# Performance work log

Hardware: AMD Instinct MI355X
Metric: run time of the kernel (lower is better)

The kernel has to match this reference:

```python
import jax, jax.numpy as jnp
import numpy as np

HEADS = 8
DIM_HEAD = 64
C = 512              # in_channels == inner_dim = heads*dim_head
WIN = 7              # window size implied by rel_pos table (2*7-1 = 13)
EPS = 1e-5


def setup_inputs() -> dict:
    key = jax.random.key(0)
    ks = jax.random.split(key, 6)
    B = 2048
    inner = HEADS * DIM_HEAD
    x = jax.random.normal(ks[0], (B, C, WIN, WIN), dtype=jnp.float32)
    gamma = jnp.ones((C,), dtype=jnp.float32)
    beta = jnp.zeros((C,), dtype=jnp.float32)
    w_qkv = jax.random.normal(ks[1], (C, 3 * inner), dtype=jnp.float32) / np.sqrt(C)
    rel_table = jax.random.normal(ks[2], (2 * WIN - 1, 2 * WIN - 1, HEADS), dtype=jnp.float32)
    w_out = jax.random.normal(ks[3], (inner, C), dtype=jnp.float32) / np.sqrt(inner)
    b_out = jnp.zeros((C,), dtype=jnp.float32)
    return {"x": x, "gamma": gamma, "beta": beta, "w_qkv": w_qkv,
            "rel_table": rel_table, "w_out": w_out, "b_out": b_out}


def _rel_pos_bias(rel_table, H, W):
    # Swin-style additive bias: bias[h, i, j] = table[hi-hj+H-1, wi-wj+W-1, h]
    hh = jnp.arange(H)
    ww = jnp.arange(W)
    hi = jnp.repeat(hh, W)          # [N] row index of each flattened position
    wi = jnp.tile(ww, H)            # [N] col index
    dh = hi[:, None] - hi[None, :] + (H - 1)   # [N, N]
    dw = wi[:, None] - wi[None, :] + (W - 1)   # [N, N]
    bias = rel_table[dh, dw]        # [N, N, heads]
    return jnp.transpose(bias, (2, 0, 1))      # [heads, N, N]


def reference(x, gamma, beta, w_qkv, rel_table, w_out, b_out):
    B, Cc, H, W = x.shape
    N = H * W
    shortcut = x
    xs = jnp.transpose(x.reshape(B, Cc, N), (0, 2, 1))   # [B, N, C]
    # LayerNorm over channel dim
    mu = jnp.mean(xs, axis=-1, keepdims=True)
    var = jnp.var(xs, axis=-1, keepdims=True)
    xn = (xs - mu) * jax.lax.rsqrt(var + EPS) * gamma + beta
    qkv = xn @ w_qkv                                      # [B, N, 3*inner]
    q, k, v = jnp.split(qkv, 3, axis=-1)
    def heads(t):
        return jnp.transpose(t.reshape(B, N, HEADS, DIM_HEAD), (0, 2, 1, 3))  # [B,h,N,d]
    q, k, v = heads(q), heads(k), heads(v)
    scale = DIM_HEAD ** -0.5
    dots = jnp.einsum('bhnd,bhmd->bhnm', q, k) * scale   # [B,h,N,N]
    dots = dots + _rel_pos_bias(rel_table, H, W)[None]   # add Swin-style bias
    attn = jax.nn.softmax(dots, axis=-1)
    out = jnp.einsum('bhnm,bhmd->bhnd', attn, v)         # [B,h,N,d]
    out = jnp.transpose(out, (0, 2, 1, 3)).reshape(B, N, HEADS * DIM_HEAD)
    out = out @ w_out + b_out                            # [B, N, C]
    out = jnp.transpose(out, (0, 2, 1)).reshape(B, Cc, H, W)
    return out + shortcut
```

## Files before the change

### kernel.cpp

```cpp
#include <hip/hip_runtime.h>

#define BATCH 2048
#define CH 512
#define NTOK 49
#define NHEAD 8
#define DHEAD 64

typedef __attribute__((ext_vector_type(8))) short bf16x8;
typedef __attribute__((ext_vector_type(4))) float f32x4;

__device__ __forceinline__ ushort f2bf(float f) {
  union { float f; unsigned u; } v; v.f = f;
  unsigned r = v.u + 0x7fffu + ((v.u >> 16) & 1u);
  return (ushort)(r >> 16);
}

__device__ __forceinline__ float bf2f(ushort u) {
  union { unsigned u; float f; } v; v.u = ((unsigned)u) << 16;
  return v.f;
}

#define MFMA16(a, b, c) __builtin_amdgcn_mfma_f32_16x16x32_bf16((a), (b), (c), 0, 0, 0)

#define GLOAD_LDS16(gsrc, ldst)                                                  \
  __builtin_amdgcn_global_load_lds((const __attribute__((address_space(1))) void*)(gsrc), \
                                   (__attribute__((address_space(3))) void*)(ldst), 16, 0, 0)

__global__ void prep_kernel(const float* __restrict__ w_qkv, const float* __restrict__ w_out,
                            const float* __restrict__ rel, ushort* __restrict__ wqkvB,
                            ushort* __restrict__ woutF, float* __restrict__ biasF) {
  int tid = blockIdx.x * blockDim.x + threadIdx.x;
  int stride = gridDim.x * blockDim.x;
  for (int i = tid; i < 12 * 16 * 8 * 64 * 8; i += stride) {
    int j = i & 7, lane = (i >> 3) & 63, cbs = (i >> 9) & 7, kk = (i >> 12) & 15, nb = i >> 16;
    int o = nb * 128 + cbs * 16 + (lane & 15);
    int c = kk * 32 + (lane >> 4) * 8 + j;
    wqkvB[i] = f2bf(w_qkv[c * 1536 + o]);
  }
  for (int i = tid; i < 32 * 16 * 64 * 8; i += stride) {
    int j = i & 7, lane = (i >> 3) & 63, ks = (i >> 9) & 15, cb = i >> 13;
    int o = cb * 16 + (lane & 15);
    int c = ks * 32 + (lane >> 4) * 8 + j;
    woutF[i] = f2bf(w_out[c * 512 + o]);
  }
  for (int i = tid; i < NHEAD * 4 * 4 * 64; i += stride) {
    int lane = i & 63, nt = (i >> 6) & 3, mt = (i >> 8) & 3, h = i >> 10;
    int cc = lane & 15, g = lane >> 4;
    float4 v;
#pragma unroll
    for (int r = 0; r < 4; r++) {
      int n = mt * 16 + 4 * g + r;
      int m = nt * 16 + cc;
      float bv = -1e30f;
      if (n < NTOK && m < NTOK) {
        int dh = n / 7 - m / 7 + 6;
        int dw = n % 7 - m % 7 + 6;
        bv = rel[(dh * 13 + dw) * 8 + h];
      }
      ((float*)&v)[r] = bv;
    }
    ((float4*)biasF)[i] = v;
  }
}

__global__ __launch_bounds__(256) void ln_kernel(const float* __restrict__ x,
                                                 const float* __restrict__ gamma,
                                                 const float* __restrict__ beta,
                                                 ushort* __restrict__ xnW) {
  int b = blockIdx.x;
  int t = threadIdx.x;
  __shared__ ushort xsb[CH][NTOK];
  __shared__ float muL[64], rsL[64];
  const float4* x4 = (const float4*)(x + (size_t)b * CH * NTOK);
  for (int i4 = t; i4 < CH * NTOK / 4; i4 += 256) {
    float4 v = x4[i4];
    int lf = i4 * 4;
#pragma unroll
    for (int e = 0; e < 4; e++) {
      int idx = lf + e;
      int c = idx / NTOK, n = idx - c * NTOK;
      xsb[c][n] = f2bf(((const float*)&v)[e]);
    }
  }
  __syncthreads();
  int row = t >> 2, sub = t & 3;
  float s = 0.f, s2 = 0.f;
  if (row < NTOK) {
    for (int c = sub; c < CH; c += 4) {
      float v = bf2f(xsb[c][row]);
      s += v;
      s2 += v * v;
    }
  }
  s += __shfl_xor(s, 1);
  s += __shfl_xor(s, 2);
  s2 += __shfl_xor(s2, 1);
  s2 += __shfl_xor(s2, 2);
  if (sub == 0 && row < NTOK) {
    float m = s * (1.f / CH);
    muL[row] = m;
    rsL[row] = rsqrtf(s2 * (1.f / CH) - m * m + 1e-5f);
  }
  __syncthreads();
  ushort* dst = xnW + (size_t)b * NTOK * CH;
  for (int i = t; i < NTOK * 64; i += 256) {
    int n = i >> 6, c0 = (i & 63) * 8;
    float mu = muL[n], rs = rsL[n];
    ushort tmp[8];
#pragma unroll
    for (int j = 0; j < 8; j++) {
      int c = c0 + j;
      tmp[j] = f2bf((bf2f(xsb[c][n]) - mu) * rs * gamma[c] + beta[c]);
    }
    *(uint4*)(dst + (size_t)n * CH + c0) = *(const uint4*)tmp;
  }
}

__global__ __launch_bounds__(256, 4) void qkv_gemm(const ushort* __restrict__ xnW,
                                                   const ushort* __restrict__ wqkvB,
                                                   ushort* __restrict__ qW,
                                                   ushort* __restrict__ kW,
                                                   ushort* __restrict__ vW) {
  int bid = blockIdx.x;
  int f = (bid & 7) * 1176 + (bid >> 3);
  int mb = f / 12, nb = f - mb * 12;
  int r0 = mb * 128;
  int t = threadIdx.x, lane = t & 63, w = t >> 6;
  int wm = w >> 1, wn = w & 1;

  __shared__ __align__(16) ushort lds[16384];

  const int arow = lane & 15, g = lane >> 4;
  const ushort* wBbase = wqkvB + (size_t)nb * 16 * 4096;
  const ushort* xbase = xnW + (size_t)r0 * CH;

  int drow = t >> 3;
  int slot = t & 7;
  int gchunk = slot ^ (drow & 7);

#pragma unroll
  for (int i = 0; i < 4; i++) {
    int row = drow + i * 32;
    GLOAD_LDS16(xbase + (size_t)row * CH + gchunk * 8, lds + i * 2048 + t * 8);
  }
  __syncthreads();

  f32x4 acc[4][4];
#pragma unroll
  for (int mt = 0; mt < 4; mt++)
#pragma unroll
    for (int nt = 0; nt < 4; nt++) acc[mt][nt] = (f32x4){0.f, 0.f, 0.f, 0.f};

  int cur = 0;
  for (int stage = 0; stage < 8; ++stage) {
    if (stage < 7) {
      int nxt = cur ^ 1, kk = stage + 1;
#pragma unroll
      for (int i = 0; i < 4; i++) {
        GLOAD_LDS16(xbase + (size_t)(drow + i * 32) * CH + kk * 64 + gchunk * 8,
                    lds + nxt * 8192 + i * 2048 + t * 8);
      }
    }
    const ushort* lA = lds + cur * 8192;
#pragma unroll
    for (int ks = 0; ks < 2; ks++) {
      int kk2 = stage * 2 + ks;
      const ushort* wp = wBbase + (size_t)kk2 * 4096 + (wn * 4) * 512 + lane * 8;
      bf16x8 bfr[4];
#pragma unroll
      for (int nt = 0; nt < 4; nt++) bfr[nt] = *(const bf16x8*)(wp + nt * 512);
      bf16x8 afr[4];
#pragma unroll
      for (int mt = 0; mt < 4; mt++) {
        int row = wm * 64 + mt * 16 + arow;
        afr[mt] = *(const bf16x8*)&lA[row * 64 + ((ks * 4 + g) ^ (arow & 7)) * 8];
      }
#pragma unroll
      for (int mt = 0; mt < 4; mt++)
#pragma unroll
        for (int nt = 0; nt < 4; nt++) acc[mt][nt] = MFMA16(afr[mt], bfr[nt], acc[mt][nt]);
    }
    __syncthreads();
    cur ^= 1;
  }

  ushort(*oL)[136] = (ushort(*)[136])lds;
  int h0 = (nb & 3) * 2;
  int sct = nb >> 2;
  float sc = (sct == 0) ? 0.125f : 1.0f;
#pragma unroll
  for (int hh = 0; hh < 2; hh++) {
    if (wm == hh) {
#pragma unroll
      for (int mt = 0; mt < 4; mt++)
#pragma unroll
        for (int nt = 0; nt < 4; nt++)
#pragma unroll
          for (int r = 0; r < 4; r++) {
            int rn = mt * 16 + 4 * g + r;
            oL[rn][wn * 64 + nt * 16 + arow] = f2bf(acc[mt][nt][r] * sc);
          }
    }
    __syncthreads();
    if (sct < 2) {
      ushort* dst = (sct == 0 ? qW : kW);
      for (int i = t; i < 64 * 16; i += 256) {
        int rn = i >> 4, c8 = i & 15;
        int grow = r0 + hh * 64 + rn;
        int b = grow / 49, n = grow - b * 49;
        int h = h0 + (c8 >> 3);
        *(uint4*)(dst + (size_t)(b * 8 + h) * (NTOK * 64) + n * 64 + (c8 & 7) * 8) =
            *(const uint4*)&oL[rn][c8 * 8];
      }
    } else {
      for (int i = t; i < 64 * 128; i += 256) {
        int rn = i & 63, col = i >> 6;
        int grow = r0 + hh * 64 + rn;
        int b = grow / 49, n = grow - b * 49;
        int h = h0 + (col >> 6), d = col & 63;
        vW[(size_t)(b * 8 + h) * 4096 + d * 64 + n] = oL[rn][col];
      }
    }
    __syncthreads();
  }
}

__global__ __launch_bounds__(512, 3) void attnproj(const ushort* __restrict__ qW,
                                                   const ushort* __restrict__ kW,
                                                   const ushort* __restrict__ vW,
                                                   const float* __restrict__ biasF,
                                                   const ushort* __restrict__ woutF,
                                                   const float* __restrict__ b_out,
                                                   const float* __restrict__ x,
                                                   float* __restrict__ out) {
  int b = blockIdx.x;
  int t = threadIdx.x;
  int lane = t & 63;
  int w = t >> 6;

  __shared__ __align__(16) ushort lds[25480];
  ushort* plb = lds + w * 3136;

  const int c = lane & 15, g = lane >> 4;
  const ushort* qb = qW + (size_t)(b * 8 + w) * NTOK * 64;
  const ushort* kb = kW + (size_t)(b * 8 + w) * NTOK * 64;
  const ushort* vb = vW + (size_t)(b * 8 + w) * 64 * 64;
  const float4* bf = (const float4*)biasF + (size_t)w * 16 * 64;

  f32x4 s[4][4];
#pragma unroll
  for (int mt = 0; mt < 4; mt++)
#pragma unroll
    for (int nt = 0; nt < 4; nt++) s[mt][nt] = (f32x4){0.f, 0.f, 0.f, 0.f};
  __builtin_amdgcn_s_setprio(1);
#pragma unroll
  for (int ks = 0; ks < 2; ks++) {
    bf16x8 kf[4];
#pragma unroll
    for (int nt = 0; nt < 4; nt++)
      kf[nt] = *(const bf16x8*)(kb + (size_t)(nt * 16 + c) * 64 + ks * 32 + g * 8);
#pragma unroll
    for (int mt = 0; mt < 4; mt++) {
      bf16x8 qf = *(const bf16x8*)(qb + (size_t)(mt * 16 + c) * 64 + ks * 32 + g * 8);
#pragma unroll
      for (int nt = 0; nt < 4; nt++) s[mt][nt] = MFMA16(qf, kf[nt], s[mt][nt]);
    }
  }
  __builtin_amdgcn_s_setprio(0);

#pragma unroll
  for (int mt = 0; mt < 4; mt++)
#pragma unroll
    for (int nt = 0; nt < 4; nt++) {
      float4 bb = bf[(mt * 4 + nt) * 64 + lane];
#pragma unroll
      for (int r = 0; r < 4; r++) s[mt][nt][r] += ((const float*)&bb)[r];
    }

#pragma unroll
  for (int mt = 0; mt < 4; mt++)
#pragma unroll
    for (int r = 0; r < 4; r++) {
      float mx = fmaxf(fmaxf(s[mt][0][r], s[mt][1][r]), fmaxf(s[mt][2][r], s[mt][3][r]));
      mx = fmaxf(mx, __shfl_xor(mx, 1));
      mx = fmaxf(mx, __shfl_xor(mx, 2));
      mx = fmaxf(mx, __shfl_xor(mx, 4));
      mx = fmaxf(mx, __shfl_xor(mx, 8));
      float p0 = __expf(s[mt][0][r] - mx);
      float p1 = __expf(s[mt][1][r] - mx);
      float p2 = __expf(s[mt][2][r] - mx);
      float p3 = __expf(s[mt][3][r] - mx);
      float sum = p0 + p1 + p2 + p3;
      sum += __shfl_xor(sum, 1);
      sum += __shfl_xor(sum, 2);
      sum += __shfl_xor(sum, 4);
      sum += __shfl_xor(sum, 8);
      float rinv = 1.f / sum;
      int n = mt * 16 + 4 * g + r;
      if (n < NTOK) {
        int n7 = n & 7;
        int chi = c >> 3, clo = c & 7;
        plb[n * 64 + ((0 + chi) ^ n7) * 8 + clo] = f2bf(p0 * rinv);
        plb[n * 64 + ((2 + chi) ^ n7) * 8 + clo] = f2bf(p1 * rinv);
        plb[n * 64 + ((4 + chi) ^ n7) * 8 + clo] = f2bf(p2 * rinv);
        plb[n * 64 + ((6 + chi) ^ n7) * 8 + clo] = f2bf(p3 * rinv);
      }
    }

  f32x4 o[4][4];
#pragma unroll
  for (int mt = 0; mt < 4; mt++)
#pragma unroll
    for (int nt = 0; nt < 4; nt++) o[mt][nt] = (f32x4){0.f, 0.f, 0.f, 0.f};
  __builtin_amdgcn_s_setprio(1);
#pragma unroll
  for (int ks = 0; ks < 2; ks++) {
    bf16x8 vf[4];
#pragma unroll
    for (int nt = 0; nt < 4; nt++)
      vf[nt] = *(const bf16x8*)(vb + (size_t)(nt * 16 + c) * 64 + ks * 32 + g * 8);
#pragma unroll
    for (int mt = 0; mt < 4; mt++) {
      int row = mt * 16 + c;
      int rr = row < NTOK ? row : 48;
      bf16x8 pf = *(const bf16x8*)&plb[rr * 64 + ((ks * 4 + g) ^ (rr & 7)) * 8];
#pragma unroll
      for (int nt = 0; nt < 4; nt++) o[mt][nt] = MFMA16(pf, vf[nt], o[mt][nt]);
    }
  }
  __builtin_amdgcn_s_setprio(0);

  bf16x8 bcur[4];
#pragma unroll
  for (int nt = 0; nt < 4; nt++)
    bcur[nt] = *(const bf16x8*)(woutF + ((size_t)((w * 4 + nt) * 16 + 0)) * 512 + lane * 8);

  __syncthreads();

  ushort(*aoL)[520] = (ushort(*)[520])lds;
#pragma unroll
  for (int mt = 0; mt < 4; mt++)
#pragma unroll
    for (int nt = 0; nt < 4; nt++)
#pragma unroll
      for (int r = 0; r < 4; r++) {
        int n = mt * 16 + 4 * g + r;
        if (n < NTOK) aoL[n][w * 64 + nt * 16 + c] = f2bf(o[mt][nt][r]);
      }
  __syncthreads();

  f32x4 pacc[4][4];
#pragma unroll
  for (int mt = 0; mt < 4; mt++)
#pragma unroll
    for (int nt = 0; nt < 4; nt++) pacc[mt][nt] = (f32x4){0.f, 0.f, 0.f, 0.f};
#pragma unroll
  for (int step = 0; step < 16; step++) {
    bf16x8 bnxt[4];
    if (step < 15) {
#pragma unroll
      for (int nt = 0; nt < 4; nt++)
        bnxt[nt] = *(const bf16x8*)(woutF + ((size_t)((w * 4 + nt) * 16 + step + 1)) * 512 + lane * 8);
    }
    bf16x8 afr[4];
#pragma unroll
    for (int mt = 0; mt < 4; mt++) {
      int row = mt * 16 + c;
      int rr = row < NTOK ? row : 48;
      afr[mt] = *(const bf16x8*)&aoL[rr][step * 32 + g * 8];
    }
    __builtin_amdgcn_s_setprio(1);
#pragma unroll
    for (int mt = 0; mt < 4; mt++)
#pragma unroll
      for (int nt = 0; nt < 4; nt++) pacc[mt][nt] = MFMA16(afr[mt], bcur[nt], pacc[mt][nt]);
    __builtin_amdgcn_s_setprio(0);
#pragma unroll
    for (int nt = 0; nt < 4; nt++) bcur[nt] = bnxt[nt];
  }

  float(*oL)[260] = (float(*)[260])lds;
  for (int half = 0; half < 2; half++) {
    __syncthreads();
    if ((w >> 2) == half) {
      int wl = w & 3;
#pragma unroll
      for (int mt = 0; mt < 4; mt++)
#pragma unroll
        for (int nt = 0; nt < 4; nt++)
#pragma unroll
          for (int r = 0; r < 4; r++) {
            int rn = mt * 16 + 4 * g + r;
            if (rn < NTOK) oL[rn][wl * 64 + nt * 16 + c] = pacc[mt][nt][r];
          }
    }
    __syncthreads();
    int c0 = half * 256;
    const float4* x4 = (const float4*)(x + ((size_t)b * CH + c0) * NTOK);
    float4* o4 = (float4*)(out + ((size_t)b * CH + c0) * NTOK);
    const float* bo = b_out + c0;
    for (int i = t; i < 3136; i += 512) {
      float4 xv = x4[i];
      float4 ov;
      int lf = i * 4;
#pragma unroll
      for (int e = 0; e < 4; e++) {
        int cl = (lf + e) / NTOK, n = (lf + e) - cl * NTOK;
        ((float*)&ov)[e] = oL[n][cl] + bo[cl] + ((const float*)&xv)[e];
      }
      o4[i] = ov;
    }
  }
}

extern "C" void kernel_launch(void* const* d_in, const int* in_sizes, int n_in,
                              void* d_out, int out_size, void* d_ws, size_t ws_size,
                              hipStream_t stream) {
  const float* x = (const float*)d_in[0];
  const float* gamma = (const float*)d_in[1];
  const float* beta = (const float*)d_in[2];
  const float* w_qkv = (const float*)d_in[3];
  const float* rel = (const float*)d_in[4];
  const float* w_out = (const float*)d_in[5];
  const float* b_out = (const float*)d_in[6];
  float* out = (float*)d_out;

  char* ws = (char*)d_ws;
  size_t off = 0;
  ushort* wqkvB = (ushort*)(ws + off); off += (size_t)12 * 16 * 4096 * 2;
  ushort* woutF = (ushort*)(ws + off); off += (size_t)512 * 512 * 2;
  float* biasF = (float*)(ws + off);   off += (size_t)NHEAD * 16 * 64 * 4 * 4;
  ushort* qW = (ushort*)(ws + off);    off += ((size_t)BATCH * 8 * NTOK * 64 + 1024) * 2;
  ushort* kW = (ushort*)(ws + off);    off += ((size_t)BATCH * 8 * NTOK * 64 + 1024) * 2;
  ushort* vW = (ushort*)(ws + off);    off += (size_t)BATCH * 8 * 64 * 64 * 2;
  ushort* xnW = (ushort*)(ws + off);   off += (size_t)BATCH * NTOK * CH * 2;
  (void)ws_size;

  prep_kernel<<<1024, 256, 0, stream>>>(w_qkv, w_out, rel, wqkvB, woutF, biasF);
  ln_kernel<<<BATCH, 256, 0, stream>>>(x, gamma, beta, xnW);
  qkv_gemm<<<784 * 12, 256, 0, stream>>>(xnW, wqkvB, qW, kW, vW);
  attnproj<<<BATCH, 512, 0, stream>>>(qW, kW, vW, biasF, woutF, b_out, x, out);
}
```

Before: 552.4 us.

## Triple-buffer QKV GEMM A tiles and register-prefetch B fragments one stage ahead

Restructures the QKV projection GEMM main loop into a fully unrolled three-stage software pipeline. A tiles in LDS are prefetched two stages ahead, and weight (B) fragments are prefetched into alternating register sets one stage ahead. Explicit vmcnt waits plus a raw barrier replace the per-stage __syncthreads. The aim is to hide global-load latency behind MFMA work. In exchange it uses more LDS and registers, and lowers launch_bounds occupancy from 4 to 3 blocks per CU. The hand-set vmcnt counts are fragile if the compiler reorders the loads.

```diff
diff --git a/kernel.cpp b/kernel.cpp
--- a/kernel.cpp
+++ b/kernel.cpp
@@ -116,7 +116,42 @@
   }
 }
 
-__global__ __launch_bounds__(256, 4) void qkv_gemm(const ushort* __restrict__ xnW,
+#define QKV_PROLOGUE_STAGE(S)                                                    \
+  _Pragma("unroll") for (int i = 0; i < 4; i++)                                  \
+      GLOAD_LDS16(xbase + (size_t)(drow + i * 32) * CH + (S) * 64 + gchunk * 8,  \
+                  lds + (S) * 8192 + i * 2048 + t * 8);
+
+#define QKV_BLOAD(DST, S)                                                        \
+  {                                                                              \
+    const ushort* wp_ = wBbase + (size_t)(S) * 8192 + (wn * 4) * 512 + lane * 8; \
+    _Pragma("unroll") for (int q_ = 0; q_ < 8; q_++)                             \
+        DST[q_] = *(const bf16x8*)(wp_ + (q_ >> 2) * 4096 + (q_ & 3) * 512);     \
+  }
+
+#define QKV_STAGE(S, VMC, BCUR, BNXT)                                            \
+  {                                                                              \
+    asm volatile("s_waitcnt vmcnt(" VMC ")" ::: "memory");                       \
+    __builtin_amdgcn_s_barrier();                                                \
+    if ((S) + 2 < 8) {                                                           \
+      _Pragma("unroll") for (int i = 0; i < 4; i++)                              \
+          GLOAD_LDS16(xbase + (size_t)(drow + i * 32) * CH + ((S) + 2) * 64 + gchunk * 8, \
+                      lds + (((S) + 2) % 3) * 8192 + i * 2048 + t * 8);          \
+    }                                                                            \
+    if ((S) + 1 < 8) QKV_BLOAD(BNXT, (S) + 1)                                    \
+    const ushort* lA_ = lds + ((S) % 3) * 8192;                                  \
+    _Pragma("unroll") for (int ks = 0; ks < 2; ks++) {                           \
+      bf16x8 afr_[4];                                                            \
+      _Pragma("unroll") for (int mt = 0; mt < 4; mt++) {                         \
+        int row_ = wm * 64 + mt * 16 + arow;                                     \
+        afr_[mt] = *(const bf16x8*)&lA_[row_ * 64 + ((ks * 4 + g) ^ (arow & 7)) * 8]; \
+      }                                                                          \
+      _Pragma("unroll") for (int mt = 0; mt < 4; mt++)                           \
+        _Pragma("unroll") for (int nt = 0; nt < 4; nt++)                         \
+            acc[mt][nt] = MFMA16(afr_[mt], BCUR[ks * 4 + nt], acc[mt][nt]);      \
+    }                                                                            \
+  }
+
+__global__ __launch_bounds__(256, 3) void qkv_gemm(const ushort* __restrict__ xnW,
                                                    const ushort* __restrict__ wqkvB,
                                                    ushort* __restrict__ qW,
                                                    ushort* __restrict__ kW,
@@ -128,7 +163,7 @@
   int t = threadIdx.x, lane = t & 63, w = t >> 6;
   int wm = w >> 1, wn = w & 1;
 
-  __shared__ __align__(16) ushort lds[16384];
+  __shared__ __align__(16) ushort lds[24576];
 
   const int arow = lane & 15, g = lane >> 4;
   const ushort* wBbase = wqkvB + (size_t)nb * 16 * 4096;
@@ -138,51 +173,25 @@
   int slot = t & 7;
   int gchunk = slot ^ (drow & 7);
 
-#pragma unroll
-  for (int i = 0; i < 4; i++) {
-    int row = drow + i * 32;
-    GLOAD_LDS16(xbase + (size_t)row * CH + gchunk * 8, lds + i * 2048 + t * 8);
-  }
+  f32x4 acc[4][4];
+#pragma unroll
+  for (int mt = 0; mt < 4; mt++)
+#pragma unroll
+    for (int nt = 0; nt < 4; nt++) acc[mt][nt] = (f32x4){0.f, 0.f, 0.f, 0.f};
+
+  bf16x8 bA[8], bB[8];
+  QKV_PROLOGUE_STAGE(0)
+  QKV_PROLOGUE_STAGE(1)
+  QKV_BLOAD(bA, 0)
+  QKV_STAGE(0, "12", bA, bB)
+  QKV_STAGE(1, "20", bB, bA)
+  QKV_STAGE(2, "20", bA, bB)
+  QKV_STAGE(3, "20", bB, bA)
+  QKV_STAGE(4, "20", bA, bB)
+  QKV_STAGE(5, "20", bB, bA)
+  QKV_STAGE(6, "20", bA, bB)
+  QKV_STAGE(7, "16", bB, bA)
   __syncthreads();
-
-  f32x4 acc[4][4];
-#pragma unroll
-  for (int mt = 0; mt < 4; mt++)
-#pragma unroll
-    for (int nt = 0; nt < 4; nt++) acc[mt][nt] = (f32x4){0.f, 0.f, 0.f, 0.f};
-
-  int cur = 0;
-  for (int stage = 0; stage < 8; ++stage) {
-    if (stage < 7) {
-      int nxt = cur ^ 1, kk = stage + 1;
-#pragma unroll
-      for (int i = 0; i < 4; i++) {
-        GLOAD_LDS16(xbase + (size_t)(drow + i * 32) * CH + kk * 64 + gchunk * 8,
-                    lds + nxt * 8192 + i * 2048 + t * 8);
-      }
-    }
-    const ushort* lA = lds + cur * 8192;
-#pragma unroll
-    for (int ks = 0; ks < 2; ks++) {
-      int kk2 = stage * 2 + ks;
-      const ushort* wp = wBbase + (size_t)kk2 * 4096 + (wn * 4) * 512 + lane * 8;
-      bf16x8 bfr[4];
-#pragma unroll
-      for (int nt = 0; nt < 4; nt++) bfr[nt] = *(const bf16x8*)(wp + nt * 512);
-      bf16x8 afr[4];
-#pragma unroll
-      for (int mt = 0; mt < 4; mt++) {
-        int row = wm * 64 + mt * 16 + arow;
-        afr[mt] = *(const bf16x8*)&lA[row * 64 + ((ks * 4 + g) ^ (arow & 7)) * 8];
-      }
-#pragma unroll
-      for (int mt = 0; mt < 4; mt++)
-#pragma unroll
-        for (int nt = 0; nt < 4; nt++) acc[mt][nt] = MFMA16(afr[mt], bfr[nt], acc[mt][nt]);
-    }
-    __syncthreads();
-    cur ^= 1;
-  }
 
   ushort(*oL)[136] = (ushort(*)[136])lds;
   int h0 = (nb & 3) * 2;
```

Result: no change. 551.4 us (-0.2%).
